# Optimization experiments

Measured on AMD Instinct MI355X. Metric: run time of the kernel, lower is better.

The kernel has to match this reference:

```python
import jax, jax.numpy as jnp
import numpy as np

NUM_GRAPHS = 64
NEG_SLOPE = 0.2  # DGL GATConv default negative_slope


def _gat_layer(h, W, a_l, a_r, b, src, dst, n_nodes):
    # DGL GATConv, num_heads=1: feat = h @ W (no bias in fc),
    # e_ij = LeakyReLU(a_l . feat_src + a_r . feat_dst), softmax over incoming
    # edges of each dst node, out_dst = sum alpha * feat_src + bias.
    feat = h @ W                      # [N, D]
    el = feat @ a_l                   # [N]
    er = feat @ a_r                   # [N]
    e = jax.nn.leaky_relu(el[src] + er[dst], NEG_SLOPE)   # [E]
    m = jax.ops.segment_max(e, dst, num_segments=n_nodes)  # per-dst max
    ex = jnp.exp(e - m[dst])
    s = jax.ops.segment_sum(ex, dst, num_segments=n_nodes)
    alpha = ex / s[dst]               # edge softmax
    out = jax.ops.segment_sum(feat[src] * alpha[:, None], dst, num_segments=n_nodes)
    return out + b


def setup_inputs() -> dict:
    key = jax.random.key(0)
    ks = jax.random.split(key, 12)
    N, E, D_IN, D_H, C = 100000, 1600000, 128, 128, 2
    h = jax.random.normal(ks[0], (N, D_IN), dtype=jnp.float32)
    src = jax.random.randint(ks[1], (E,), 0, N)
    dst = jax.random.randint(ks[2], (E,), 0, N)
    graph_id = jnp.sort(jax.random.randint(ks[3], (N,), 0, NUM_GRAPHS))
    sc = 1.0 / np.sqrt(D_IN)
    params = {
        'W1': jax.random.normal(ks[4], (D_IN, D_H), dtype=jnp.float32) * sc,
        'al1': jax.random.normal(ks[5], (D_H,), dtype=jnp.float32) * sc,
        'ar1': jax.random.normal(ks[6], (D_H,), dtype=jnp.float32) * sc,
        'b1': jnp.zeros((D_H,), dtype=jnp.float32),
        'W2': jax.random.normal(ks[7], (D_H, D_H), dtype=jnp.float32) * sc,
        'al2': jax.random.normal(ks[8], (D_H,), dtype=jnp.float32) * sc,
        'ar2': jax.random.normal(ks[9], (D_H,), dtype=jnp.float32) * sc,
        'b2': jnp.zeros((D_H,), dtype=jnp.float32),
        'Wfc': jax.random.normal(ks[10], (D_H, C), dtype=jnp.float32) * sc,
        'bfc': jnp.zeros((C,), dtype=jnp.float32),
    }
    return dict(h=h, src=src, dst=dst, graph_id=graph_id, **params)


def reference(h, src, dst, graph_id, W1, al1, ar1, b1, W2, al2, ar2, b2, Wfc, bfc):
    n_nodes = h.shape[0]
    x = jax.nn.relu(_gat_layer(h, W1, al1, ar1, b1, src, dst, n_nodes))
    x = jax.nn.relu(_gat_layer(x, W2, al2, ar2, b2, src, dst, n_nodes))
    # dgl.mean_nodes over the batched graph
    counts = jax.ops.segment_sum(jnp.ones((n_nodes,), x.dtype), graph_id,
                                 num_segments=NUM_GRAPHS)
    hg = jax.ops.segment_sum(x, graph_id, num_segments=NUM_GRAPHS)
    hg = hg / jnp.clip(counts, 1.0)[:, None]          # [G, D]
    logits = hg @ Wfc + bfc                            # [G, C]
    return jax.nn.log_softmax(logits, axis=-1)
```

## Files before the change

kernel.cpp:

```cpp
#include <hip/hip_runtime.h>
#include <math.h>

#define NUM_GRAPHS 64
#define D 128
#define MT 64
#define ETILE 4096
#define PCH 16
#define CAP 3072

typedef __attribute__((ext_vector_type(8))) short bf16x8;
typedef __attribute__((ext_vector_type(4))) float f32x4;
typedef __attribute__((ext_vector_type(2))) float f32x2;

#if defined(__has_builtin)
#if __has_builtin(__builtin_amdgcn_cvt_pk_f32_fp8) && __has_builtin(__builtin_amdgcn_cvt_pk_fp8_f32)
#define HW_FP8 1
#endif
#endif
#ifndef HW_FP8
#define HW_FP8 0
#endif

__device__ __forceinline__ unsigned bf16rne(float x) {
    unsigned u = __float_as_uint(x);
    return (u + 0x7fffu + ((u >> 16) & 1u)) >> 16;
}
__device__ __forceinline__ float bflo(unsigned u) { return __uint_as_float(u << 16); }
__device__ __forceinline__ float bfhi(unsigned u) { return __uint_as_float(u & 0xffff0000u); }

__device__ __forceinline__ unsigned encf(float f) {
    unsigned u = __float_as_uint(f);
    return (u & 0x80000000u) ? ~u : (u | 0x80000000u);
}
__device__ __forceinline__ float decf(unsigned e) {
    unsigned u = (e & 0x80000000u) ? (e & 0x7fffffffu) : ~e;
    return __uint_as_float(u);
}

#if !HW_FP8
__device__ __forceinline__ unsigned fp8_enc1(float f) {
    unsigned u = __float_as_uint(f);
    unsigned s = (u >> 24) & 0x80u;
    float a = fabsf(f);
    if (a >= 448.f) return s | 0x7Eu;
    if (a < 0.0009765625f) return s;
    if (a < 0.015625f) {
        int m = (int)rintf(a * 512.f);
        if (m > 7) return s | 0x08u;
        return s | (unsigned)m;
    }
    unsigned au = u & 0x7FFFFFFFu;
    unsigned r = au + 0x000FFFFFu + ((au >> 20) & 1u);
    unsigned code = (((r >> 23) - 120u) << 3) | ((r >> 20) & 7u);
    if (code > 0x7Eu) code = 0x7Eu;
    return s | code;
}
__device__ __forceinline__ float fp8_dec1(unsigned b) {
    unsigned ef = b & 0x7Fu;
    unsigned e = ef >> 3, m = ef & 7u;
    float mag = (e == 0) ? (float)m * 1.953125e-3f
                         : __uint_as_float(((e + 120u) << 23) | (m << 20));
    return (b & 0x80u) ? -mag : mag;
}
#endif

__device__ __forceinline__ unsigned fp8pk4(float f0, float f1, float f2, float f3) {
#if HW_FP8
    int d = __builtin_amdgcn_cvt_pk_fp8_f32(f0, f1, 0, false);
    d = __builtin_amdgcn_cvt_pk_fp8_f32(f2, f3, d, true);
    return (unsigned)d;
#else
    return fp8_enc1(f0) | (fp8_enc1(f1) << 8) | (fp8_enc1(f2) << 16) | (fp8_enc1(f3) << 24);
#endif
}

__device__ __forceinline__ void fma_bf16(const uint4& q, float w,
                                         f32x2& a0, f32x2& a1, f32x2& a2, f32x2& a3) {
    f32x2 f;
    f.x = bflo(q.x); f.y = bfhi(q.x); a0 += w * f;
    f.x = bflo(q.y); f.y = bfhi(q.y); a1 += w * f;
    f.x = bflo(q.z); f.y = bfhi(q.z); a2 += w * f;
    f.x = bflo(q.w); f.y = bfhi(q.w); a3 += w * f;
}
__device__ __forceinline__ void fma_fp8(const uint2& q, float w,
                                        f32x2& a0, f32x2& a1, f32x2& a2, f32x2& a3) {
#if HW_FP8
    f32x2 p;
    p = __builtin_amdgcn_cvt_pk_f32_fp8((int)q.x, false); a0 += w * p;
    p = __builtin_amdgcn_cvt_pk_f32_fp8((int)q.x, true);  a1 += w * p;
    p = __builtin_amdgcn_cvt_pk_f32_fp8((int)q.y, false); a2 += w * p;
    p = __builtin_amdgcn_cvt_pk_f32_fp8((int)q.y, true);  a3 += w * p;
#else
    f32x2 p;
    p.x = fp8_dec1(q.x & 0xFFu);         p.y = fp8_dec1((q.x >> 8) & 0xFFu);  a0 += w * p;
    p.x = fp8_dec1((q.x >> 16) & 0xFFu); p.y = fp8_dec1(q.x >> 24);           a1 += w * p;
    p.x = fp8_dec1(q.y & 0xFFu);         p.y = fp8_dec1((q.y >> 8) & 0xFFu);  a2 += w * p;
    p.x = fp8_dec1((q.y >> 16) & 0xFFu); p.y = fp8_dec1(q.y >> 24);           a3 += w * p;
#endif
}

__device__ __forceinline__ void gload_lds16(const void* g, void* l) {
    __builtin_amdgcn_global_load_lds(
        (const __attribute__((address_space(1))) void*)g,
        (__attribute__((address_space(3))) void*)l, 16, 0, 0);
}


__global__ __launch_bounds__(256) void k_partition(
    const int* __restrict__ src, const int* __restrict__ dst,
    int* __restrict__ bcnt, unsigned* __restrict__ part, int E, int nbT,
    const float* __restrict__ W1, const float* __restrict__ W2,
    unsigned short* __restrict__ Wt1, unsigned short* __restrict__ Wt2,
    const int* __restrict__ gid, int* __restrict__ gs, int* __restrict__ ge, int N) {
    int b = blockIdx.x;
    int tid = threadIdx.x;
    if (b < nbT) {
        __shared__ int h[1024];
        __shared__ int cur[1024];
        for (int i = tid; i < 1024; i += 256) h[i] = 0;
        __syncthreads();
        int e0 = b * ETILE;
        int e1 = min(e0 + ETILE, E);
        for (int i = e0 + tid; i < e1; i += 256) atomicAdd(&h[dst[i] >> 7], 1);
        __syncthreads();
        for (int i = tid; i < 1024; i += 256) {
            int c = h[i];
            cur[i] = c ? atomicAdd(&bcnt[i], c) : 0;
        }
        __syncthreads();
        for (int i = e0 + tid; i < e1; i += 256) {
            int d = dst[i];
            int bk = d >> 7;
            int pos = atomicAdd(&cur[bk], 1);
            if (pos < CAP)
                part[(size_t)bk * CAP + pos] = (unsigned)src[i] | ((unsigned)(d & 127) << 17);
        }
    } else if (b < nbT + 16) {
        int bb = b - nbT;
        const float* W = (bb & 8) ? W2 : W1;
        unsigned short* Wt = (bb & 8) ? Wt2 : Wt1;
        int n = (bb & 7) * 16 + (tid >> 4);
        int c = tid & 15;
        unsigned v[8];
        #pragma unroll
        for (int j = 0; j < 8; ++j) v[j] = bf16rne(W[(c * 8 + j) * D + n]);
        uint4 pk;
        pk.x = v[0] | (v[1] << 16);
        pk.y = v[2] | (v[3] << 16);
        pk.z = v[4] | (v[5] << 16);
        pk.w = v[6] | (v[7] << 16);
        ((uint4*)Wt)[n * 16 + c] = pk;
    } else {
        int n = (b - nbT - 16) * 256 + tid;
        if (n >= N) return;
        int g = gid[n];
        if (n == 0 || gid[n - 1] != g) gs[g] = n + 1;
        if (n == N - 1 || gid[n + 1] != g) ge[g] = n + 1;
    }
}


__global__ __launch_bounds__(256) void k_gemm_mfma_sort(
    const void* __restrict__ Xv, int x_fp32,
    const unsigned short* __restrict__ Wt16,
    const float* __restrict__ al, const float* __restrict__ ar,
    unsigned short* __restrict__ feat16, unsigned char* __restrict__ feat8, int out_fp8,
    float* __restrict__ el, float* __restrict__ er,
    unsigned* __restrict__ glmax_u, int N, int gemmBlocks,
    const unsigned* __restrict__ part, const int* __restrict__ bcnt,
    int2* __restrict__ rbe, int* __restrict__ csr_src) {
    __shared__ uint4 WsU[128 * 16];
    __shared__ float smax[4];
    int bx = blockIdx.x;
    int T = gridDim.x;
    int g0 = (int)((long long)bx * gemmBlocks / T);
    int g1 = (int)((long long)(bx + 1) * gemmBlocks / T);
    int tid = threadIdx.x;

    if (g1 == g0) {
        int b = bx - g0;
        int base = b * CAP;
        int bcnt_b = min(bcnt[b], CAP);
        int* ldeg = (int*)WsU;
        int* lcur = ldeg + 128;
        if (tid < 128) ldeg[tid] = 0;
        __syncthreads();
        for (int i = tid; i < bcnt_b; i += 256)
            atomicAdd(&ldeg[part[(size_t)base + i] >> 17], 1);
        __syncthreads();
        int myv = (tid < 128) ? ldeg[tid] : 0;
        for (int off = 1; off < 128; off <<= 1) {
            int y = 0;
            if (tid < 128 && tid >= off) y = ldeg[tid - off];
            __syncthreads();
            if (tid < 128) ldeg[tid] += y;
            __syncthreads();
        }
        if (tid < 128) {
            int excl = ldeg[tid] - myv;
            int node = (b << 7) + tid;
            if (node < N) rbe[node] = make_int2(base + excl, base + excl + myv);
            lcur[tid] = base + excl;
        }
        __syncthreads();
        for (int i = tid; i < bcnt_b; i += 256) {
            unsigned v = part[(size_t)base + i];
            int pos = atomicAdd(&lcur[v >> 17], 1);
            csr_src[pos] = (int)(v & 0x1FFFFu);
        }
        return;
    }

    int row0 = g0 * MT;
    int w = tid >> 6, lane = tid & 63;
    int quad = lane >> 4, l16 = lane & 15;

    #pragma unroll
    for (int k = 0; k < 8; ++k) {
        int s = w * 512 + k * 64 + lane;
        int n = s >> 4, cc = (s & 15) ^ (n & 15);
        gload_lds16((const uint4*)Wt16 + n * 16 + cc, &WsU[w * 512 + k * 64]);
    }

    int arow = row0 + w * 16 + l16;
    int arowc = (arow < N) ? arow : (N - 1);
    bf16x8 A[4];
    if (x_fp32) {
        const float4* X4 = (const float4*)Xv;
        #pragma unroll
        for (int ks = 0; ks < 4; ++ks) {
            int c = ks * 4 + quad;
            float4 f0 = X4[(size_t)arowc * 32 + c * 2];
            float4 f1 = X4[(size_t)arowc * 32 + c * 2 + 1];
            uint4 o;
            o.x = bf16rne(f0.x) | (bf16rne(f0.y) << 16);
            o.y = bf16rne(f0.z) | (bf16rne(f0.w) << 16);
            o.z = bf16rne(f1.x) | (bf16rne(f1.y) << 16);
            o.w = bf16rne(f1.z) | (bf16rne(f1.w) << 16);
            A[ks] = *(const bf16x8*)&o;
        }
    } else {
        const bf16x8* X8 = (const bf16x8*)Xv;
        #pragma unroll
        for (int ks = 0; ks < 4; ++ks)
            A[ks] = X8[(size_t)arowc * 16 + ks * 4 + quad];
    }
    __syncthreads();

    const bf16x8* WsF = (const bf16x8*)WsU;
    f32x4 acc[8];
    #pragma unroll
    for (int i = 0; i < 8; ++i) acc[i] = (f32x4){0.f, 0.f, 0.f, 0.f};

    #pragma unroll
    for (int ks = 0; ks < 4; ++ks) {
        int c = ks * 4 + quad;
        #pragma unroll
        for (int nt = 0; nt < 8; ++nt) {
            bf16x8 B = WsF[((nt * 16 + l16) << 4) | (c ^ l16)];
            acc[nt] = __builtin_amdgcn_mfma_f32_16x16x32_bf16(A[ks], B, acc[nt], 0, 0, 0);
        }
    }

    float alv[8], arv[8];
    #pragma unroll
    for (int nt = 0; nt < 8; ++nt) { alv[nt] = al[nt * 16 + l16]; arv[nt] = ar[nt * 16 + l16]; }
    float lmax = -1e30f;
    #pragma unroll
    for (int r = 0; r < 4; ++r) {
        float pl = 0.f, pr = 0.f;
        #pragma unroll
        for (int nt = 0; nt < 8; ++nt) { pl += acc[nt][r] * alv[nt]; pr += acc[nt][r] * arv[nt]; }
        #pragma unroll
        for (int o = 1; o < 16; o <<= 1) { pl += __shfl_xor(pl, o); pr += __shfl_xor(pr, o); }
        int row = row0 + w * 16 + quad * 4 + r;
        if (l16 == 0 && row < N) { el[row] = pl; er[row] = pr; }
        lmax = fmaxf(lmax, pl);
    }
    lmax = fmaxf(lmax, __shfl_xor(lmax, 16));
    lmax = fmaxf(lmax, __shfl_xor(lmax, 32));
    if (lane == 0) smax[w] = lmax;

    __syncthreads();
    unsigned short* WsS = (unsigned short*)WsU;
    #pragma unroll
    for (int nt = 0; nt < 8; ++nt)
        #pragma unroll
        for (int r = 0; r < 4; ++r) {
            int lrow = w * 16 + quad * 4 + r;
            int col = nt * 16 + l16;
            int ch = col >> 3;
            int sc = ch ^ (lrow & 15);
            WsS[lrow * 128 + sc * 8 + (col & 7)] = (unsigned short)bf16rne(acc[nt][r]);
        }
    __syncthreads();
    if (tid == 0) {
        float bm = fmaxf(fmaxf(smax[0], smax[1]), fmaxf(smax[2], smax[3]));
        atomicMax(glmax_u, encf(bm));
    }
    if (out_fp8) {
        for (int idx = tid; idx < MT * 16; idx += 256) {
            int n = idx >> 4, c = idx & 15;
            int row = row0 + n;
            if (row < N) {
                uint4 v = WsU[(n << 4) | (c ^ (n & 15))];
                uint2 o;
                o.x = fp8pk4(bflo(v.x), bfhi(v.x), bflo(v.y), bfhi(v.y));
                o.y = fp8pk4(bflo(v.z), bfhi(v.z), bflo(v.w), bfhi(v.w));
                ((uint2*)(feat8 + (size_t)row * 128))[c] = o;
            }
        }
    } else {
        for (int idx = tid; idx < MT * 16; idx += 256) {
            int n = idx >> 4, c = idx & 15;
            int row = row0 + n;
            if (row < N) ((uint4*)feat16)[(size_t)row * 16 + c] = WsU[(n << 4) | (c ^ (n & 15))];
        }
    }
}


template <int FP8>
__global__ __launch_bounds__(256) void k_aggregate(
    const void* __restrict__ featv, const float* __restrict__ el,
    const float* __restrict__ er, const int2* __restrict__ rbe,
    const int* __restrict__ csr_src, const float* __restrict__ bias,
    const unsigned* __restrict__ glmax_u, unsigned short* __restrict__ outv,
    const int* __restrict__ gid, int dopool, float* __restrict__ hgpart,
    int* __restrict__ gtag, float* __restrict__ hg_extra, int N) {
    __shared__ float bacc[4][16][8];
    __shared__ int gsm[4];
    int tid = threadIdx.x;
    int wv = tid >> 6;
    int lane = tid & 63;
    int wid = blockIdx.x * 4 + wv;
    bool act = wid < N;

    int beg = 0, end = 0;
    float erd = 0.f;
    if (act) { int2 be = rbe[wid]; beg = be.x; end = be.y; erd = er[wid]; }
    float M = decf(glmax_u[0]) + erd;
    M = fmaxf(M, 0.2f * M);

    int qa = lane >> 4, sub = lane & 15;
    const char* fb = (const char*)featv + (FP8 ? (sub << 3) : (sub << 4));
    f32x2 a0 = {0.f, 0.f}, a1 = {0.f, 0.f}, a2 = {0.f, 0.f}, a3 = {0.f, 0.f};
    float s = 0.f;
    int j = beg + qa;
    for (; j + 12 < end; j += 16) {
        int jb = j - qa;
        int iw = jb + sub; iw = (iw < end) ? iw : (end - 1);
        int snw = csr_src[iw];
        int sn0 = csr_src[j], sn1 = csr_src[j + 4];
        int sn2 = csr_src[j + 8], sn3 = csr_src[j + 12];
        float tw = el[snw] + erd;
        if constexpr (FP8) {
            uint2 q0 = *(const uint2*)(fb + ((unsigned)sn0 << 7));
            uint2 q1 = *(const uint2*)(fb + ((unsigned)sn1 << 7));
            uint2 q2 = *(const uint2*)(fb + ((unsigned)sn2 << 7));
            uint2 q3 = *(const uint2*)(fb + ((unsigned)sn3 << 7));
            tw = fmaxf(tw, 0.2f * tw);
            float ww = __expf(tw - M);
            float w0 = __shfl(ww, qa);
            float w1 = __shfl(ww, qa + 4);
            float w2 = __shfl(ww, qa + 8);
            float w3 = __shfl(ww, qa + 12);
            s += (w0 + w1) + (w2 + w3);
            fma_fp8(q0, w0, a0, a1, a2, a3);
            fma_fp8(q1, w1, a0, a1, a2, a3);
            fma_fp8(q2, w2, a0, a1, a2, a3);
            fma_fp8(q3, w3, a0, a1, a2, a3);
        } else {
            uint4 q0 = *(const uint4*)(fb + ((unsigned)sn0 << 8));
            uint4 q1 = *(const uint4*)(fb + ((unsigned)sn1 << 8));
            uint4 q2 = *(const uint4*)(fb + ((unsigned)sn2 << 8));
            uint4 q3 = *(const uint4*)(fb + ((unsigned)sn3 << 8));
            tw = fmaxf(tw, 0.2f * tw);
            float ww = __expf(tw - M);
            float w0 = __shfl(ww, qa);
            float w1 = __shfl(ww, qa + 4);
            float w2 = __shfl(ww, qa + 8);
            float w3 = __shfl(ww, qa + 12);
            s += (w0 + w1) + (w2 + w3);
            fma_bf16(q0, w0, a0, a1, a2, a3);
            fma_bf16(q1, w1, a0, a1, a2, a3);
            fma_bf16(q2, w2, a0, a1, a2, a3);
            fma_bf16(q3, w3, a0, a1, a2, a3);
        }
    }
    for (; j + 4 < end; j += 8) {
        int sn0 = csr_src[j], sn1 = csr_src[j + 4];
        float t0 = el[sn0] + erd, t1 = el[sn1] + erd;
        if constexpr (FP8) {
            uint2 q0 = *(const uint2*)(fb + ((unsigned)sn0 << 7));
            uint2 q1 = *(const uint2*)(fb + ((unsigned)sn1 << 7));
            t0 = fmaxf(t0, 0.2f * t0); t1 = fmaxf(t1, 0.2f * t1);
            float w0 = __expf(t0 - M), w1 = __expf(t1 - M);
            s += w0 + w1;
            fma_fp8(q0, w0, a0, a1, a2, a3);
            fma_fp8(q1, w1, a0, a1, a2, a3);
        } else {
            uint4 q0 = *(const uint4*)(fb + ((unsigned)sn0 << 8));
            uint4 q1 = *(const uint4*)(fb + ((unsigned)sn1 << 8));
            t0 = fmaxf(t0, 0.2f * t0); t1 = fmaxf(t1, 0.2f * t1);
            float w0 = __expf(t0 - M), w1 = __expf(t1 - M);
            s += w0 + w1;
            fma_bf16(q0, w0, a0, a1, a2, a3);
            fma_bf16(q1, w1, a0, a1, a2, a3);
        }
    }
    if (j < end) {
        int sn = csr_src[j];
        float t = el[sn] + erd;
        t = fmaxf(t, 0.2f * t);
        float w = __expf(t - M);
        s += w;
        if constexpr (FP8) {
            uint2 q = *(const uint2*)(fb + ((unsigned)sn << 7));
            fma_fp8(q, w, a0, a1, a2, a3);
        } else {
            uint4 q = *(const uint4*)(fb + ((unsigned)sn << 8));
            fma_bf16(q, w, a0, a1, a2, a3);
        }
    }
    float vr[8] = {a0.x, a0.y, a1.x, a1.y, a2.x, a2.y, a3.x, a3.y};
    #pragma unroll
    for (int c = 0; c < 8; ++c) {
        vr[c] += __shfl_xor(vr[c], 16);
        vr[c] += __shfl_xor(vr[c], 32);
    }
    s += __shfl_xor(s, 16);
    s += __shfl_xor(s, 32);
    float inv = (end > beg) ? 1.f / s : 0.f;

    if (dopool) {
        if (lane < 16) {
            float4 b0 = ((const float4*)bias)[lane * 2];
            float4 b1 = ((const float4*)bias)[lane * 2 + 1];
            float* bw = bacc[wv][lane];
            bw[0] = fmaxf(vr[0] * inv + b0.x, 0.f);
            bw[1] = fmaxf(vr[1] * inv + b0.y, 0.f);
            bw[2] = fmaxf(vr[2] * inv + b0.z, 0.f);
            bw[3] = fmaxf(vr[3] * inv + b0.w, 0.f);
            bw[4] = fmaxf(vr[4] * inv + b1.x, 0.f);
            bw[5] = fmaxf(vr[5] * inv + b1.y, 0.f);
            bw[6] = fmaxf(vr[6] * inv + b1.z, 0.f);
            bw[7] = fmaxf(vr[7] * inv + b1.w, 0.f);
        }
        if (lane == 0) gsm[wv] = act ? gid[wid] : -1;
        __syncthreads();
        int g0 = gsm[0];
        bool uni = (gsm[1] == g0) && (gsm[2] == g0) && (gsm[3] == g0) && (g0 >= 0);
        if (tid < 128) {
            int sb = tid >> 3, k = tid & 7;
            if (uni) {
                float sum = bacc[0][sb][k] + bacc[1][sb][k] + bacc[2][sb][k] + bacc[3][sb][k];
                hgpart[(size_t)blockIdx.x * D + tid] = sum;
            } else {
                #pragma unroll
                for (int u = 0; u < 4; ++u) {
                    int g = gsm[u];
                    if (g >= 0) atomicAdd(&hg_extra[g * D + tid], bacc[u][sb][k]);
                }
            }
        }
        if (tid == 0) gtag[blockIdx.x] = uni ? g0 : -1;
    } else if (act && lane < 16) {
        float4 b0 = ((const float4*)bias)[lane * 2];
        float4 b1 = ((const float4*)bias)[lane * 2 + 1];
        float v[8];
        v[0] = fmaxf(vr[0] * inv + b0.x, 0.f);
        v[1] = fmaxf(vr[1] * inv + b0.y, 0.f);
        v[2] = fmaxf(vr[2] * inv + b0.z, 0.f);
        v[3] = fmaxf(vr[3] * inv + b0.w, 0.f);
        v[4] = fmaxf(vr[4] * inv + b1.x, 0.f);
        v[5] = fmaxf(vr[5] * inv + b1.y, 0.f);
        v[6] = fmaxf(vr[6] * inv + b1.z, 0.f);
        v[7] = fmaxf(vr[7] * inv + b1.w, 0.f);
        uint4 pk;
        pk.x = bf16rne(v[0]) | (bf16rne(v[1]) << 16);
        pk.y = bf16rne(v[2]) | (bf16rne(v[3]) << 16);
        pk.z = bf16rne(v[4]) | (bf16rne(v[5]) << 16);
        pk.w = bf16rne(v[6]) | (bf16rne(v[7]) << 16);
        ((uint4*)outv)[(size_t)wid * 16 + lane] = pk;
    }
}


__global__ __launch_bounds__(128) void k_poolreduce(
    const float* __restrict__ hgpart, const int* __restrict__ gtag,
    const int* __restrict__ gs, const int* __restrict__ ge,
    float* __restrict__ hg_extra) {
    int g = blockIdx.x;
    int d = threadIdx.x;
    int s = gs[g] - 1, e = ge[g] - 1;
    if (s < 0 || e < s) return;
    int b0 = s >> 2, b1 = e >> 2;
    float acc = 0.f;
    for (int b = b0 + (int)blockIdx.y; b <= b1; b += PCH) {
        int t = gtag[b];
        float v = hgpart[(size_t)b * D + d];
        acc += (t == g) ? v : 0.f;
    }
    if (acc != 0.f) atomicAdd(&hg_extra[g * D + d], acc);
}


__global__ void k_final(const float* __restrict__ hg, const int* __restrict__ gs,
                        const int* __restrict__ ge, const float* __restrict__ Wfc,
                        const float* __restrict__ bfc, float* __restrict__ out) {
    int g = threadIdx.x;
    if (g >= NUM_GRAPHS) return;
    int start = gs[g] - 1, last = ge[g] - 1;
    float cnt = (start >= 0 && start <= last) ? (float)(last - start + 1) : 1.f;
    float ic = 1.f / cnt;
    float l0 = bfc[0], l1 = bfc[1];
    for (int d = 0; d < D; d++) {
        float v = hg[g * D + d] * ic;
        l0 += v * Wfc[2 * d];
        l1 += v * Wfc[2 * d + 1];
    }
    float mm = fmaxf(l0, l1);
    float lse = mm + logf(expf(l0 - mm) + expf(l1 - mm));
    out[2 * g] = l0 - lse;
    out[2 * g + 1] = l1 - lse;
}


extern "C" void kernel_launch(void* const* d_in, const int* in_sizes, int n_in,
                              void* d_out, int out_size, void* d_ws, size_t ws_size,
                              hipStream_t stream) {
    const float* h   = (const float*)d_in[0];
    const int* src   = (const int*)d_in[1];
    const int* dst   = (const int*)d_in[2];
    const int* gid   = (const int*)d_in[3];
    const float* W1  = (const float*)d_in[4];
    const float* al1 = (const float*)d_in[5];
    const float* ar1 = (const float*)d_in[6];
    const float* b1  = (const float*)d_in[7];
    const float* W2  = (const float*)d_in[8];
    const float* al2 = (const float*)d_in[9];
    const float* ar2 = (const float*)d_in[10];
    const float* b2  = (const float*)d_in[11];
    const float* Wfc = (const float*)d_in[12];
    const float* bfc = (const float*)d_in[13];
    float* out = (float*)d_out;

    int N = in_sizes[0] / D;
    int E = in_sizes[1];
    int NB = (N + 127) >> 7;
    int nbW = (N + 3) / 4;

    char* p = (char*)d_ws;
    unsigned short* feat16  = (unsigned short*)p; p += (size_t)N * D * 2;
    unsigned char* feat8 = (unsigned char*)feat16;
    unsigned short* featAgg = (unsigned short*)p; p += (size_t)N * D * 2;
    float* el    = (float*)p; p += (size_t)N * 4;
    float* er    = (float*)p; p += (size_t)N * 4;
    int2* rbe    = (int2*)p;  p += (size_t)N * 8;
    int* csr_src = (int*)p;   p += (size_t)NB * CAP * 4;
    size_t partBytes = (size_t)NB * CAP * 4;
    size_t hgpBytes  = (size_t)nbW * D * 4;
    unsigned* part = (unsigned*)p;
    float* hgpart  = (float*)p;
    p += (partBytes > hgpBytes) ? partBytes : hgpBytes;
    int* bcnt    = (int*)p;   p += 1028 * 4;
    unsigned* glmaxu = (unsigned*)p; p += 4 * 4;
    float* hg_extra = (float*)p; p += NUM_GRAPHS * D * 4;
    int* gs      = (int*)p;   p += NUM_GRAPHS * 4;
    int* ge      = (int*)p;   p += NUM_GRAPHS * 4;
    size_t zbytes = (char*)p - (char*)bcnt;
    int* gtag    = (int*)p;   p += (size_t)nbW * 4;
    unsigned short* Wt1 = (unsigned short*)p; p += D * D * 2;
    unsigned short* Wt2 = (unsigned short*)p; p += D * D * 2;

    int nbN = (N + 255) / 256;
    int nbT = (E + ETILE - 1) / ETILE;
    int gemmB = (N + MT - 1) / MT;

    hipMemsetAsync(bcnt, 0, zbytes, stream);

    k_partition<<<nbT + 16 + nbN, 256, 0, stream>>>(src, dst, bcnt, part, E, nbT,
                                                    W1, W2, Wt1, Wt2, gid, gs, ge, N);

    k_gemm_mfma_sort<<<gemmB + NB, 256, 0, stream>>>(
        h, 1, Wt1, al1, ar1, feat16, feat8, 1, el, er, glmaxu, N, gemmB,
        part, bcnt, rbe, csr_src);
    k_aggregate<1><<<nbW, 256, 0, stream>>>(feat8, el, er, rbe, csr_src,
                                            b1, glmaxu, featAgg, gid, 0,
                                            hgpart, gtag, hg_extra, N);

    k_gemm_mfma_sort<<<gemmB, 256, 0, stream>>>(
        featAgg, 0, Wt2, al2, ar2, feat16, feat8, 1, el, er, glmaxu + 1, N, gemmB,
        part, bcnt, rbe, csr_src);
    k_aggregate<1><<<nbW, 256, 0, stream>>>(feat8, el, er, rbe, csr_src,
                                            b2, glmaxu + 1, nullptr, gid, 1,
                                            hgpart, gtag, hg_extra, N);

    k_poolreduce<<<dim3(NUM_GRAPHS, PCH), 128, 0, stream>>>(hgpart, gtag, gs, ge,
                                                            hg_extra);
    k_final<<<1, 64, 0, stream>>>(hg_extra, gs, ge, Wfc, bfc, out);
}
```

Baseline: 314.3 us.

## Move edge partition into first GEMM launch and split CSR sort into own kernel

Measured after the change: 333.1 us. +6.0%, slower.

```diff
diff --git a/kernel.cpp b/kernel.cpp
--- a/kernel.cpp
+++ b/kernel.cpp
@@ -74,14 +74,6 @@
 #endif
 }
 
-__device__ __forceinline__ void fma_bf16(const uint4& q, float w,
-                                         f32x2& a0, f32x2& a1, f32x2& a2, f32x2& a3) {
-    f32x2 f;
-    f.x = bflo(q.x); f.y = bfhi(q.x); a0 += w * f;
-    f.x = bflo(q.y); f.y = bfhi(q.y); a1 += w * f;
-    f.x = bflo(q.z); f.y = bfhi(q.z); a2 += w * f;
-    f.x = bflo(q.w); f.y = bfhi(q.w); a3 += w * f;
-}
 __device__ __forceinline__ void fma_fp8(const uint2& q, float w,
                                         f32x2& a0, f32x2& a1, f32x2& a2, f32x2& a3) {
 #if HW_FP8
@@ -106,17 +98,54 @@
 }
 
 
-__global__ __launch_bounds__(256) void k_partition(
-    const int* __restrict__ src, const int* __restrict__ dst,
-    int* __restrict__ bcnt, unsigned* __restrict__ part, int E, int nbT,
+__global__ __launch_bounds__(256) void k_prep(
     const float* __restrict__ W1, const float* __restrict__ W2,
     unsigned short* __restrict__ Wt1, unsigned short* __restrict__ Wt2,
     const int* __restrict__ gid, int* __restrict__ gs, int* __restrict__ ge, int N) {
     int b = blockIdx.x;
     int tid = threadIdx.x;
-    if (b < nbT) {
-        __shared__ int h[1024];
-        __shared__ int cur[1024];
+    if (b < 16) {
+        const float* W = (b & 8) ? W2 : W1;
+        unsigned short* Wt = (b & 8) ? Wt2 : Wt1;
+        int n = (b & 7) * 16 + (tid >> 4);
+        int c = tid & 15;
+        unsigned v[8];
+        #pragma unroll
+        for (int j = 0; j < 8; ++j) v[j] = bf16rne(W[(c * 8 + j) * D + n]);
+        uint4 pk;
+        pk.x = v[0] | (v[1] << 16);
+        pk.y = v[2] | (v[3] << 16);
+        pk.z = v[4] | (v[5] << 16);
+        pk.w = v[6] | (v[7] << 16);
+        ((uint4*)Wt)[n * 16 + c] = pk;
+    } else {
+        int n = (b - 16) * 256 + tid;
+        if (n >= N) return;
+        int g = gid[n];
+        if (n == 0 || gid[n - 1] != g) gs[g] = n + 1;
+        if (n == N - 1 || gid[n + 1] != g) ge[g] = n + 1;
+    }
+}
+
+
+__global__ __launch_bounds__(256) void k_gemm(
+    const void* __restrict__ Xv, int x_fp32,
+    const unsigned short* __restrict__ Wt16,
+    const float* __restrict__ al, const float* __restrict__ ar,
+    unsigned char* __restrict__ feat8,
+    float* __restrict__ el, float* __restrict__ er,
+    unsigned* __restrict__ glmax_u, int N, int gemmBlocks,
+    const int* __restrict__ src, const int* __restrict__ dst,
+    int* __restrict__ bcnt, unsigned* __restrict__ part, int E) {
+    __shared__ uint4 WsU[128 * 16];
+    __shared__ float smax[4];
+    int bx = blockIdx.x;
+    int tid = threadIdx.x;
+
+    if (bx >= gemmBlocks) {
+        int b = bx - gemmBlocks;
+        int* h = (int*)WsU;
+        int* cur = h + 1024;
         for (int i = tid; i < 1024; i += 256) h[i] = 0;
         __syncthreads();
         int e0 = b * ETILE;
@@ -135,83 +164,10 @@
             if (pos < CAP)
                 part[(size_t)bk * CAP + pos] = (unsigned)src[i] | ((unsigned)(d & 127) << 17);
         }
-    } else if (b < nbT + 16) {
-        int bb = b - nbT;
-        const float* W = (bb & 8) ? W2 : W1;
-        unsigned short* Wt = (bb & 8) ? Wt2 : Wt1;
-        int n = (bb & 7) * 16 + (tid >> 4);
-        int c = tid & 15;
-        unsigned v[8];
-        #pragma unroll
-        for (int j = 0; j < 8; ++j) v[j] = bf16rne(W[(c * 8 + j) * D + n]);
-        uint4 pk;
-        pk.x = v[0] | (v[1] << 16);
-        pk.y = v[2] | (v[3] << 16);
-        pk.z = v[4] | (v[5] << 16);
-        pk.w = v[6] | (v[7] << 16);
-        ((uint4*)Wt)[n * 16 + c] = pk;
-    } else {
-        int n = (b - nbT - 16) * 256 + tid;
-        if (n >= N) return;
-        int g = gid[n];
-        if (n == 0 || gid[n - 1] != g) gs[g] = n + 1;
-        if (n == N - 1 || gid[n + 1] != g) ge[g] = n + 1;
-    }
-}
-
-
-__global__ __launch_bounds__(256) void k_gemm_mfma_sort(
-    const void* __restrict__ Xv, int x_fp32,
-    const unsigned short* __restrict__ Wt16,
-    const float* __restrict__ al, const float* __restrict__ ar,
-    unsigned short* __restrict__ feat16, unsigned char* __restrict__ feat8, int out_fp8,
-    float* __restrict__ el, float* __restrict__ er,
-    unsigned* __restrict__ glmax_u, int N, int gemmBlocks,
-    const unsigned* __restrict__ part, const int* __restrict__ bcnt,
-    int2* __restrict__ rbe, int* __restrict__ csr_src) {
-    __shared__ uint4 WsU[128 * 16];
-    __shared__ float smax[4];
-    int bx = blockIdx.x;
-    int T = gridDim.x;
-    int g0 = (int)((long long)bx * gemmBlocks / T);
-    int g1 = (int)((long long)(bx + 1) * gemmBlocks / T);
-    int tid = threadIdx.x;
-
-    if (g1 == g0) {
-        int b = bx - g0;
-        int base = b * CAP;
-        int bcnt_b = min(bcnt[b], CAP);
-        int* ldeg = (int*)WsU;
-        int* lcur = ldeg + 128;
-        if (tid < 128) ldeg[tid] = 0;
-        __syncthreads();
-        for (int i = tid; i < bcnt_b; i += 256)
-            atomicAdd(&ldeg[part[(size_t)base + i] >> 17], 1);
-        __syncthreads();
-        int myv = (tid < 128) ? ldeg[tid] : 0;
-        for (int off = 1; off < 128; off <<= 1) {
-            int y = 0;
-            if (tid < 128 && tid >= off) y = ldeg[tid - off];
-            __syncthreads();
-            if (tid < 128) ldeg[tid] += y;
-            __syncthreads();
-        }
-        if (tid < 128) {
-            int excl = ldeg[tid] - myv;
-            int node = (b << 7) + tid;
-            if (node < N) rbe[node] = make_int2(base + excl, base + excl + myv);
-            lcur[tid] = base + excl;
-        }
-        __syncthreads();
-        for (int i = tid; i < bcnt_b; i += 256) {
-            unsigned v = part[(size_t)base + i];
-            int pos = atomicAdd(&lcur[v >> 17], 1);
-            csr_src[pos] = (int)(v & 0x1FFFFu);
-        }
         return;
     }
 
-    int row0 = g0 * MT;
+    int row0 = bx * MT;
     int w = tid >> 6, lane = tid & 63;
     int quad = lane >> 4, l16 = lane & 15;
 
@@ -298,31 +254,59 @@
         float bm = fmaxf(fmaxf(smax[0], smax[1]), fmaxf(smax[2], smax[3]));
         atomicMax(glmax_u, encf(bm));
     }
-    if (out_fp8) {
-        for (int idx = tid; idx < MT * 16; idx += 256) {
-            int n = idx >> 4, c = idx & 15;
-            int row = row0 + n;
-            if (row < N) {
-                uint4 v = WsU[(n << 4) | (c ^ (n & 15))];
-                uint2 o;
-                o.x = fp8pk4(bflo(v.x), bfhi(v.x), bflo(v.y), bfhi(v.y));
-                o.y = fp8pk4(bflo(v.z), bfhi(v.z), bflo(v.w), bfhi(v.w));
-                ((uint2*)(feat8 + (size_t)row * 128))[c] = o;
-            }
-        }
-    } else {
-        for (int idx = tid; idx < MT * 16; idx += 256) {
-            int n = idx >> 4, c = idx & 15;
-            int row = row0 + n;
-            if (row < N) ((uint4*)feat16)[(size_t)row * 16 + c] = WsU[(n << 4) | (c ^ (n & 15))];
-        }
-    }
-}
-
-
-template <int FP8>
+    for (int idx = tid; idx < MT * 16; idx += 256) {
+        int n = idx >> 4, c = idx & 15;
+        int row = row0 + n;
+        if (row < N) {
+            uint4 v = WsU[(n << 4) | (c ^ (n & 15))];
+            uint2 o;
+            o.x = fp8pk4(bflo(v.x), bfhi(v.x), bflo(v.y), bfhi(v.y));
+            o.y = fp8pk4(bflo(v.z), bfhi(v.z), bflo(v.w), bfhi(v.w));
+            ((uint2*)(feat8 + (size_t)row * 128))[c] = o;
+        }
+    }
+}
+
+
+__global__ __launch_bounds__(256) void k_sort(
+    const unsigned* __restrict__ part, const int* __restrict__ bcnt,
+    int2* __restrict__ rbe, int* __restrict__ csr_src, int N) {
+    __shared__ int ldeg[128];
+    __shared__ int lcur[128];
+    int b = blockIdx.x;
+    int tid = threadIdx.x;
+    int base = b * CAP;
+    int bcnt_b = min(bcnt[b], CAP);
+    if (tid < 128) ldeg[tid] = 0;
+    __syncthreads();
+    for (int i = tid; i < bcnt_b; i += 256)
+        atomicAdd(&ldeg[part[(size_t)base + i] >> 17], 1);
+    __syncthreads();
+    int myv = (tid < 128) ? ldeg[tid] : 0;
+    for (int off = 1; off < 128; off <<= 1) {
+        int y = 0;
+        if (tid < 128 && tid >= off) y = ldeg[tid - off];
+        __syncthreads();
+        if (tid < 128) ldeg[tid] += y;
+        __syncthreads();
+    }
+    if (tid < 128) {
+        int excl = ldeg[tid] - myv;
+        int node = (b << 7) + tid;
+        if (node < N) rbe[node] = make_int2(base + excl, base + excl + myv);
+        lcur[tid] = base + excl;
+    }
+    __syncthreads();
+    for (int i = tid; i < bcnt_b; i += 256) {
+        unsigned v = part[(size_t)base + i];
+        int pos = atomicAdd(&lcur[v >> 17], 1);
+        csr_src[pos] = (int)(v & 0x1FFFFu);
+    }
+}
+
+
 __global__ __launch_bounds__(256) void k_aggregate(
-    const void* __restrict__ featv, const float* __restrict__ el,
+    const unsigned char* __restrict__ feat8, const float* __restrict__ el,
     const float* __restrict__ er, const int2* __restrict__ rbe,
     const int* __restrict__ csr_src, const float* __restrict__ bias,
     const unsigned* __restrict__ glmax_u, unsigned short* __restrict__ outv,
@@ -343,7 +327,7 @@
     M = fmaxf(M, 0.2f * M);
 
     int qa = lane >> 4, sub = lane & 15;
-    const char* fb = (const char*)featv + (FP8 ? (sub << 3) : (sub << 4));
+    const char* fb = (const char*)feat8 + (sub << 3);
     f32x2 a0 = {0.f, 0.f}, a1 = {0.f, 0.f}, a2 = {0.f, 0.f}, a3 = {0.f, 0.f};
     float s = 0.f;
     int j = beg + qa;
@@ -354,60 +338,32 @@
         int sn0 = csr_src[j], sn1 = csr_src[j + 4];
         int sn2 = csr_src[j + 8], sn3 = csr_src[j + 12];
         float tw = el[snw] + erd;
-        if constexpr (FP8) {
-            uint2 q0 = *(const uint2*)(fb + ((unsigned)sn0 << 7));
-            uint2 q1 = *(const uint2*)(fb + ((unsigned)sn1 << 7));
-            uint2 q2 = *(const uint2*)(fb + ((unsigned)sn2 << 7));
-            uint2 q3 = *(const uint2*)(fb + ((unsigned)sn3 << 7));
-            tw = fmaxf(tw, 0.2f * tw);
-            float ww = __expf(tw - M);
-            float w0 = __shfl(ww, qa);
-            float w1 = __shfl(ww, qa + 4);
-            float w2 = __shfl(ww, qa + 8);
-            float w3 = __shfl(ww, qa + 12);
-            s += (w0 + w1) + (w2 + w3);
-            fma_fp8(q0, w0, a0, a1, a2, a3);
-            fma_fp8(q1, w1, a0, a1, a2, a3);
-            fma_fp8(q2, w2, a0, a1, a2, a3);
-            fma_fp8(q3, w3, a0, a1, a2, a3);
-        } else {
-            uint4 q0 = *(const uint4*)(fb + ((unsigned)sn0 << 8));
-            uint4 q1 = *(const uint4*)(fb + ((unsigned)sn1 << 8));
-            uint4 q2 = *(const uint4*)(fb + ((unsigned)sn2 << 8));
-            uint4 q3 = *(const uint4*)(fb + ((unsigned)sn3 << 8));
-            tw = fmaxf(tw, 0.2f * tw);
-            float ww = __expf(tw - M);
-            float w0 = __shfl(ww, qa);
-            float w1 = __shfl(ww, qa + 4);
-            float w2 = __shfl(ww, qa + 8);
-            float w3 = __shfl(ww, qa + 12);
-            s += (w0 + w1) + (w2 + w3);
-            fma_bf16(q0, w0, a0, a1, a2, a3);
-            fma_bf16(q1, w1, a0, a1, a2, a3);
-            fma_bf16(q2, w2, a0, a1, a2, a3);
-            fma_bf16(q3, w3, a0, a1, a2, a3);
-        }
+        uint2 q0 = *(const uint2*)(fb + ((unsigned)sn0 << 7));
+        uint2 q1 = *(const uint2*)(fb + ((unsigned)sn1 << 7));
+        uint2 q2 = *(const uint2*)(fb + ((unsigned)sn2 << 7));
+        uint2 q3 = *(const uint2*)(fb + ((unsigned)sn3 << 7));
+        tw = fmaxf(tw, 0.2f * tw);
+        float ww = __expf(tw - M);
+        float w0 = __shfl(ww, qa);
+        float w1 = __shfl(ww, qa + 4);
+        float w2 = __shfl(ww, qa + 8);
+        float w3 = __shfl(ww, qa + 12);
+        s += (w0 + w1) + (w2 + w3);
+        fma_fp8(q0, w0, a0, a1, a2, a3);
+        fma_fp8(q1, w1, a0, a1, a2, a3);
+        fma_fp8(q2, w2, a0, a1, a2, a3);
+        fma_fp8(q3, w3, a0, a1, a2, a3);
     }
     for (; j + 4 < end; j += 8) {
         int sn0 = csr_src[j], sn1 = csr_src[j + 4];
         float t0 = el[sn0] + erd, t1 = el[sn1] + erd;
-        if constexpr (FP8) {
-            uint2 q0 = *(const uint2*)(fb + ((unsigned)sn0 << 7));
-            uint2 q1 = *(const uint2*)(fb + ((unsigned)sn1 << 7));
-            t0 = fmaxf(t0, 0.2f * t0); t1 = fmaxf(t1, 0.2f * t1);
-            float w0 = __expf(t0 - M), w1 = __expf(t1 - M);
-            s += w0 + w1;
-            fma_fp8(q0, w0, a0, a1, a2, a3);
-            fma_fp8(q1, w1, a0, a1, a2, a3);
-        } else {
-            uint4 q0 = *(const uint4*)(fb + ((unsigned)sn0 << 8));
-            uint4 q1 = *(const uint4*)(fb + ((unsigned)sn1 << 8));
-            t0 = fmaxf(t0, 0.2f * t0); t1 = fmaxf(t1, 0.2f * t1);
-            float w0 = __expf(t0 - M), w1 = __expf(t1 - M);
-            s += w0 + w1;
-            fma_bf16(q0, w0, a0, a1, a2, a3);
-            fma_bf16(q1, w1, a0, a1, a2, a3);
-        }
+        uint2 q0 = *(const uint2*)(fb + ((unsigned)sn0 << 7));
+        uint2 q1 = *(const uint2*)(fb + ((unsigned)sn1 << 7));
+        t0 = fmaxf(t0, 0.2f * t0); t1 = fmaxf(t1, 0.2f * t1);
+        float w0 = __expf(t0 - M), w1 = __expf(t1 - M);
+        s += w0 + w1;
+        fma_fp8(q0, w0, a0, a1, a2, a3);
+        fma_fp8(q1, w1, a0, a1, a2, a3);
     }
     if (j < end) {
         int sn = csr_src[j];
@@ -415,13 +371,8 @@
         t = fmaxf(t, 0.2f * t);
         float w = __expf(t - M);
         s += w;
-        if constexpr (FP8) {
-            uint2 q = *(const uint2*)(fb + ((unsigned)sn << 7));
-            fma_fp8(q, w, a0, a1, a2, a3);
-        } else {
-            uint4 q = *(const uint4*)(fb + ((unsigned)sn << 8));
-            fma_bf16(q, w, a0, a1, a2, a3);
-        }
+        uint2 q = *(const uint2*)(fb + ((unsigned)sn << 7));
+        fma_fp8(q, w, a0, a1, a2, a3);
     }
     float vr[8] = {a0.x, a0.y, a1.x, a1.y, a2.x, a2.y, a3.x, a3.y};
     #pragma unroll
@@ -552,8 +503,7 @@
     int nbW = (N + 3) / 4;
 
     char* p = (char*)d_ws;
-    unsigned short* feat16  = (unsigned short*)p; p += (size_t)N * D * 2;
-    unsigned char* feat8 = (unsigned char*)feat16;
+    unsigned char* feat8 = (unsigned char*)p; p += (size_t)N * D * 2;
     unsigned short* featAgg = (unsigned short*)p; p += (size_t)N * D * 2;
     float* el    = (float*)p; p += (size_t)N * 4;
     float* er    = (float*)p; p += (size_t)N * 4;
@@ -580,22 +530,22 @@
 
     hipMemsetAsync(bcnt, 0, zbytes, stream);
 
-    k_partition<<<nbT + 16 + nbN, 256, 0, stream>>>(src, dst, bcnt, part, E, nbT,
-                                                    W1, W2, Wt1, Wt2, gid, gs, ge, N);
-
-    k_gemm_mfma_sort<<<gemmB + NB, 256, 0, stream>>>(
-        h, 1, Wt1, al1, ar1, feat16, feat8, 1, el, er, glmaxu, N, gemmB,
-        part, bcnt, rbe, csr_src);
-    k_aggregate<1><<<nbW, 256, 0, stream>>>(feat8, el, er, rbe, csr_src,
-                                            b1, glmaxu, featAgg, gid, 0,
-                                            hgpart, gtag, hg_extra, N);
-
-    k_gemm_mfma_sort<<<gemmB, 256, 0, stream>>>(
-        featAgg, 0, Wt2, al2, ar2, feat16, feat8, 1, el, er, glmaxu + 1, N, gemmB,
-        part, bcnt, rbe, csr_src);
-    k_aggregate<1><<<nbW, 256, 0, stream>>>(feat8, el, er, rbe, csr_src,
-                                            b2, glmaxu + 1, nullptr, gid, 1,
-                                            hgpart, gtag, hg_extra, N);
+    k_prep<<<16 + nbN, 256, 0, stream>>>(W1, W2, Wt1, Wt2, gid, gs, ge, N);
+
+    k_gemm<<<gemmB + nbT, 256, 0, stream>>>(
+        h, 1, Wt1, al1, ar1, feat8, el, er, glmaxu, N, gemmB,
+        src, dst, bcnt, part, E);
+    k_sort<<<NB, 256, 0, stream>>>(part, bcnt, rbe, csr_src, N);
+    k_aggregate<<<nbW, 256, 0, stream>>>(feat8, el, er, rbe, csr_src,
+                                         b1, glmaxu, featAgg, gid, 0,
+                                         hgpart, gtag, hg_extra, N);
+
+    k_gemm<<<gemmB, 256, 0, stream>>>(
+        featAgg, 0, Wt2, al2, ar2, feat8, el, er, glmaxu + 1, N, gemmB,
+        src, dst, bcnt, part, E);
+    k_aggregate<<<nbW, 256, 0, stream>>>(feat8, el, er, rbe, csr_src,
+                                         b2, glmaxu + 1, nullptr, gid, 1,
+                                         hgpart, gtag, hg_extra, N);
 
     k_poolreduce<<<dim3(NUM_GRAPHS, PCH), 128, 0, stream>>>(hgpart, gtag, gs, ge,
                                                             hg_extra);
```
